# Kernel optimization log

Hardware: AMD Instinct MI355X
Metric: run time of the kernel (lower is better)

Reference implementation:

```python
import jax, jax.numpy as jnp
import numpy as np

# Static graph layout: B equal-size graphs so per-graph k is static under jit.
B = 64          # number of graphs
N_PER = 1024    # nodes per graph
RATIO = 0.5
K = max(1, int(RATIO * N_PER))  # 512 nodes kept per graph
MULTIPLIER = 1.0
N = B * N_PER   # 65536 total nodes
E = 2_097_152   # total edges
F_IN = 256
F_E = 16


def setup_inputs() -> dict:
    key = jax.random.key(0)
    k1, k2, k3, k4 = jax.random.split(key, 4)
    x = jax.random.normal(k1, (N, F_IN), dtype=jnp.float32)
    edge_index = jax.random.randint(k2, (2, E), 0, N, dtype=jnp.int32)
    edge_attr = jax.random.normal(k3, (E, F_E), dtype=jnp.float32)
    batch = jnp.repeat(jnp.arange(B, dtype=jnp.int32), N_PER)  # sorted, equal sizes
    # Linear(in_channels, 1) params (PyTorch default init style)
    W = jax.random.uniform(k4, (1, F_IN), dtype=jnp.float32,
                           minval=-1.0, maxval=1.0) / jnp.sqrt(F_IN)
    b = jnp.zeros((1,), dtype=jnp.float32)
    return {"x": x, "edge_index": edge_index, "edge_attr": edge_attr,
            "batch": batch, "W": W, "b": b}


def reference(x, edge_index, edge_attr, batch, W, b):
    # score = multiplier * tanh(proj(x))  -> [N]
    score = MULTIPLIER * jnp.tanh(x @ W.T + b)[:, 0]

    # Per-graph top-k (graphs are contiguous, equal size -> reshape + top_k)
    _, idx = jax.lax.top_k(score.reshape(B, N_PER), K)        # [B, K], desc order
    offsets = (jnp.arange(B, dtype=idx.dtype) * N_PER)[:, None]
    perm = (idx + offsets).reshape(-1)                          # [B*K] global node ids
    batch_out = jnp.repeat(jnp.arange(B, dtype=batch.dtype), K)

    # Gate kept node features by their score
    x_out = x[perm] * score[perm][:, None]                      # [B*K, F_IN]

    # filter_adj: keep edges whose both endpoints survive, remap node ids
    mask = jnp.zeros((N,), dtype=bool).at[perm].set(True)
    row, col = edge_index[0], edge_index[1]
    edge_mask = mask[row] & mask[col]                           # [E]
    node_map = jnp.zeros((N,), dtype=jnp.int32).at[perm].set(
        jnp.arange(B * K, dtype=jnp.int32))
    # jit-friendly: fixed-size outputs; invalid edges marked -1 / zeroed
    ei_new = jnp.where(edge_mask[None, :], node_map[edge_index], -1)
    ea_new = jnp.where(edge_mask[:, None], edge_attr, 0.0)

    return (x_out, ei_new, ea_new, batch_out, perm, score, edge_mask)
```

## Files before the change

kernel.cpp:

```cpp
#include <hip/hip_runtime.h>
#include <math.h>

#define BGRAPH 64
#define N_PER  1024
#define KSEL   512
#define NTOT   65536
#define EDG    2097152
#define FIN    256
#define FE     16

#define OFF_XOUT   0
#define OFF_EI     8388608
#define OFF_EA     12582912
#define OFF_BATCH  46137344
#define OFF_PERM   46170112
#define OFF_SCORE  46202880
#define OFF_EMASK  46268416

#define WS_DOTS_OFF 65536

#define GATHER_BLOCKS 8192
#define EDGE_BLOCKS   2048

__global__ __launch_bounds__(256) void score_kernel(
    const float* __restrict__ x, const float* __restrict__ W,
    const float* __restrict__ bptr, float* __restrict__ score_out,
    double* __restrict__ dot_out) {
  int wave = threadIdx.x >> 6;
  int lane = threadIdx.x & 63;
  int sub  = lane >> 4;
  int l16  = lane & 15;
  int row  = (blockIdx.x * 4 + wave) * 4 + sub;
  const float4* xr = reinterpret_cast<const float4*>(x + (size_t)row * FIN);
  const float4* wr = reinterpret_cast<const float4*>(W);
  double p = 0.0;
#pragma unroll
  for (int q = 0; q < 4; ++q) {
    float4 xv = xr[q * 16 + l16];
    float4 wv = wr[q * 16 + l16];
    p += (double)xv.x * (double)wv.x + (double)xv.y * (double)wv.y +
         (double)xv.z * (double)wv.z + (double)xv.w * (double)wv.w;
  }
#pragma unroll
  for (int off = 8; off >= 1; off >>= 1) p += __shfl_xor(p, off, 64);
  if (l16 == 0) {
    double z = p + (double)bptr[0];
    dot_out[row]   = z;
    score_out[row] = tanhf((float)z);
  }
}

__global__ __launch_bounds__(1024) void topk_kernel(
    const double* __restrict__ dots, float* __restrict__ perm_out,
    float* __restrict__ batch_out, int* __restrict__ node_map) {
  __shared__ double sk[N_PER];
  __shared__ int    si[N_PER];
  int b = blockIdx.x;
  int t = threadIdx.x;
  int base = b * N_PER;
  double key = dots[base + t];
  int    idx = t;
  node_map[base + t] = -1;
  for (int k = 2; k <= N_PER; k <<= 1) {
    for (int j = k >> 1; j > 0; j >>= 1) {
      bool lower = (t & j) == 0;
      bool dirUp = (t & k) == 0;
      double okey; int oidx;
      if (j >= 64) {
        sk[t] = key; si[t] = idx;
        __syncthreads();
        okey = sk[t ^ j]; oidx = si[t ^ j];
        __syncthreads();
      } else {
        okey = __shfl_xor(key, j, 64);
        oidx = __shfl_xor(idx, j, 64);
      }
      bool own_prec = (key > okey) || (key == okey && idx < oidx);
      bool want_prec = (lower == dirUp);
      if (own_prec != want_prec) { key = okey; idx = oidx; }
    }
  }
  if (t < KSEL) {
    int g   = base + idx;
    int gid = b * KSEL + t;
    perm_out[gid]  = (float)g;
    batch_out[gid] = (float)b;
    node_map[g]    = gid;
  }
}

__global__ __launch_bounds__(256) void tail_kernel(
    const float* __restrict__ x, const float* __restrict__ perm_f,
    const float* __restrict__ score, float* __restrict__ xout,
    const int* __restrict__ ei, const int* __restrict__ node_map,
    const float* __restrict__ ea, float* __restrict__ ei_out,
    float* __restrict__ emask_out, float* __restrict__ ea_out) {
  __shared__ float smask[1024];
  int t = threadIdx.x;

  if (blockIdx.x < GATHER_BLOCKS) {
    int wave = t >> 6;
    int lane = t & 63;
    int r = blockIdx.x * 4 + wave;
    int g = (int)perm_f[r];
    float s = score[g];
    float4 v = reinterpret_cast<const float4*>(x + (size_t)g * FIN)[lane];
    float4 o;
    o.x = v.x * s; o.y = v.y * s; o.z = v.z * s; o.w = v.w * s;
    reinterpret_cast<float4*>(xout + (size_t)r * FIN)[lane] = o;
    return;
  }

  int bid = blockIdx.x - GATHER_BLOCKS;
  int e0 = bid * 1024;
  int ft = bid * 256 + t;

  int4 r4 = reinterpret_cast<const int4*>(ei)[ft];
  int4 c4 = reinterpret_cast<const int4*>(ei + EDG)[ft];
  int nr0 = node_map[r4.x], nr1 = node_map[r4.y];
  int nr2 = node_map[r4.z], nr3 = node_map[r4.w];
  int nc0 = node_map[c4.x], nc1 = node_map[c4.y];
  int nc2 = node_map[c4.z], nc3 = node_map[c4.w];
  bool m0 = (nr0 >= 0) && (nc0 >= 0);
  bool m1 = (nr1 >= 0) && (nc1 >= 0);
  bool m2 = (nr2 >= 0) && (nc2 >= 0);
  bool m3 = (nr3 >= 0) && (nc3 >= 0);
  float4 ro = make_float4(m0 ? (float)nr0 : -1.0f, m1 ? (float)nr1 : -1.0f,
                          m2 ? (float)nr2 : -1.0f, m3 ? (float)nr3 : -1.0f);
  float4 co = make_float4(m0 ? (float)nc0 : -1.0f, m1 ? (float)nc1 : -1.0f,
                          m2 ? (float)nc2 : -1.0f, m3 ? (float)nc3 : -1.0f);
  float4 mo = make_float4(m0 ? 1.0f : 0.0f, m1 ? 1.0f : 0.0f,
                          m2 ? 1.0f : 0.0f, m3 ? 1.0f : 0.0f);
  reinterpret_cast<float4*>(ei_out)[ft]       = ro;
  reinterpret_cast<float4*>(ei_out + EDG)[ft] = co;
  reinterpret_cast<float4*>(emask_out)[ft]    = mo;
  reinterpret_cast<float4*>(smask)[t]         = mo;
  __syncthreads();

  const float4* ea4 = reinterpret_cast<const float4*>(ea) + (size_t)e0 * 4;
  float4*      out4 = reinterpret_cast<float4*>(ea_out)   + (size_t)e0 * 4;
#pragma unroll
  for (int q = 0; q < 16; ++q) {
    int fi = q * 256 + t;
    float mm = smask[fi >> 2];
    float4 v = make_float4(0.f, 0.f, 0.f, 0.f);
    if (mm != 0.0f) v = ea4[fi];
    out4[fi] = v;
  }
}

extern "C" void kernel_launch(void* const* d_in, const int* in_sizes, int n_in,
                              void* d_out, int out_size, void* d_ws, size_t ws_size,
                              hipStream_t stream) {
  const float* x  = (const float*)d_in[0];
  const int*   ei = (const int*)d_in[1];
  const float* ea = (const float*)d_in[2];
  const float* W  = (const float*)d_in[4];
  const float* bb = (const float*)d_in[5];

  float* out       = (float*)d_out;
  float* xout      = out + OFF_XOUT;
  float* ei_out    = out + OFF_EI;
  float* ea_out    = out + OFF_EA;
  float* batch_out = out + OFF_BATCH;
  float* perm_out  = out + OFF_PERM;
  float* score_out = out + OFF_SCORE;
  float* emask_out = out + OFF_EMASK;

  int*    node_map = (int*)d_ws;
  double* dots     = (double*)((int*)d_ws + WS_DOTS_OFF);

  score_kernel <<<NTOT / 16, 256, 0, stream>>>(x, W, bb, score_out, dots);
  topk_kernel  <<<BGRAPH, 1024, 0, stream>>>(dots, perm_out, batch_out, node_map);
  tail_kernel  <<<GATHER_BLOCKS + EDGE_BLOCKS, 256, 0, stream>>>(
      x, perm_out, score_out, xout, ei, node_map, ea, ei_out, emask_out, ea_out);
}
```

Measured before the change: 102.9 us.

## Sort two elements per thread in top-k and use 8 lanes per score row

The bitonic top-k now has each of 512 threads hold two adjacent elements. The j=1 stage becomes an in-register compare-swap, shuffles cover strides up to 64, and only larger strides go through shared memory, which cuts the number of block barriers. The score kernel computes each row dot product with 8 lanes instead of 16, so each block handles twice as many rows and the grid is halved. The risks are fewer threads to hide latency in the top-k and more serial work per lane in the score kernel.

```diff
diff --git a/kernel.cpp b/kernel.cpp
--- a/kernel.cpp
+++ b/kernel.cpp
@@ -28,29 +28,29 @@
     double* __restrict__ dot_out) {
   int wave = threadIdx.x >> 6;
   int lane = threadIdx.x & 63;
-  int sub  = lane >> 4;
-  int l16  = lane & 15;
-  int row  = (blockIdx.x * 4 + wave) * 4 + sub;
+  int sub  = lane >> 3;
+  int l8   = lane & 7;
+  int row  = (blockIdx.x * 4 + wave) * 8 + sub;
   const float4* xr = reinterpret_cast<const float4*>(x + (size_t)row * FIN);
   const float4* wr = reinterpret_cast<const float4*>(W);
   double p = 0.0;
 #pragma unroll
-  for (int q = 0; q < 4; ++q) {
-    float4 xv = xr[q * 16 + l16];
-    float4 wv = wr[q * 16 + l16];
+  for (int q = 0; q < 8; ++q) {
+    float4 xv = xr[q * 8 + l8];
+    float4 wv = wr[q * 8 + l8];
     p += (double)xv.x * (double)wv.x + (double)xv.y * (double)wv.y +
          (double)xv.z * (double)wv.z + (double)xv.w * (double)wv.w;
   }
 #pragma unroll
-  for (int off = 8; off >= 1; off >>= 1) p += __shfl_xor(p, off, 64);
-  if (l16 == 0) {
+  for (int off = 4; off >= 1; off >>= 1) p += __shfl_xor(p, off, 64);
+  if (l8 == 0) {
     double z = p + (double)bptr[0];
     dot_out[row]   = z;
     score_out[row] = tanhf((float)z);
   }
 }
 
-__global__ __launch_bounds__(1024) void topk_kernel(
+__global__ __launch_bounds__(512) void topk_kernel(
     const double* __restrict__ dots, float* __restrict__ perm_out,
     float* __restrict__ batch_out, int* __restrict__ node_map) {
   __shared__ double sk[N_PER];
@@ -58,34 +58,53 @@
   int b = blockIdx.x;
   int t = threadIdx.x;
   int base = b * N_PER;
-  double key = dots[base + t];
-  int    idx = t;
-  node_map[base + t] = -1;
+  int i0 = 2 * t, i1 = 2 * t + 1;
+  double k0 = dots[base + i0], k1 = dots[base + i1];
+  int id0 = i0, id1 = i1;
+  node_map[base + i0] = -1;
+  node_map[base + i1] = -1;
   for (int k = 2; k <= N_PER; k <<= 1) {
     for (int j = k >> 1; j > 0; j >>= 1) {
-      bool lower = (t & j) == 0;
-      bool dirUp = (t & k) == 0;
-      double okey; int oidx;
-      if (j >= 64) {
-        sk[t] = key; si[t] = idx;
-        __syncthreads();
-        okey = sk[t ^ j]; oidx = si[t ^ j];
-        __syncthreads();
+      if (j == 1) {
+        bool dirUp = ((i0 & k) == 0);
+        bool own_prec = (k0 > k1) || (k0 == k1 && id0 < id1);
+        if (own_prec != dirUp) {
+          double tk = k0; k0 = k1; k1 = tk;
+          int    ti = id0; id0 = id1; id1 = ti;
+        }
       } else {
-        okey = __shfl_xor(key, j, 64);
-        oidx = __shfl_xor(idx, j, 64);
+        bool lower = ((i0 & j) == 0);
+        bool dirUp = ((i0 & k) == 0);
+        bool want  = (lower == dirUp);
+        double ok0, ok1; int oid0, oid1;
+        if (j <= 64) {
+          int lx = j >> 1;
+          ok0 = __shfl_xor(k0, lx, 64);  oid0 = __shfl_xor(id0, lx, 64);
+          ok1 = __shfl_xor(k1, lx, 64);  oid1 = __shfl_xor(id1, lx, 64);
+        } else {
+          sk[i0] = k0; si[i0] = id0;
+          sk[i1] = k1; si[i1] = id1;
+          __syncthreads();
+          ok0 = sk[i0 ^ j]; oid0 = si[i0 ^ j];
+          ok1 = sk[i1 ^ j]; oid1 = si[i1 ^ j];
+          __syncthreads();
+        }
+        bool prec0 = (k0 > ok0) || (k0 == ok0 && id0 < oid0);
+        if (prec0 != want) { k0 = ok0; id0 = oid0; }
+        bool prec1 = (k1 > ok1) || (k1 == ok1 && id1 < oid1);
+        if (prec1 != want) { k1 = ok1; id1 = oid1; }
       }
-      bool own_prec = (key > okey) || (key == okey && idx < oidx);
-      bool want_prec = (lower == dirUp);
-      if (own_prec != want_prec) { key = okey; idx = oidx; }
     }
   }
-  if (t < KSEL) {
-    int g   = base + idx;
-    int gid = b * KSEL + t;
-    perm_out[gid]  = (float)g;
-    batch_out[gid] = (float)b;
-    node_map[g]    = gid;
+  if (t < KSEL / 2) {
+    int g0 = base + id0, g1 = base + id1;
+    int gid0 = b * KSEL + i0, gid1 = b * KSEL + i1;
+    perm_out[gid0]  = (float)g0;
+    perm_out[gid1]  = (float)g1;
+    batch_out[gid0] = (float)b;
+    batch_out[gid1] = (float)b;
+    node_map[g0]    = gid0;
+    node_map[g1]    = gid1;
   }
 }
 
@@ -170,8 +189,8 @@
   int*    node_map = (int*)d_ws;
   double* dots     = (double*)((int*)d_ws + WS_DOTS_OFF);
 
-  score_kernel <<<NTOT / 16, 256, 0, stream>>>(x, W, bb, score_out, dots);
-  topk_kernel  <<<BGRAPH, 1024, 0, stream>>>(dots, perm_out, batch_out, node_map);
+  score_kernel <<<NTOT / 32, 256, 0, stream>>>(x, W, bb, score_out, dots);
+  topk_kernel  <<<BGRAPH, 512, 0, stream>>>(dots, perm_out, batch_out, node_map);
   tail_kernel  <<<GATHER_BLOCKS + EDGE_BLOCKS, 256, 0, stream>>>(
       x, perm_out, score_out, xout, ei, node_map, ea, ei_out, emask_out, ea_out);
 }
```

New measurement: 106.6 us. 3.6% more time.
